# Optimization experiments

Hardware: AMD Instinct MI355X
Metric: run time of the kernel (lower is better)

Reference implementation:

```python
import jax, jax.numpy as jnp
import numpy as np

STEPS, IN_DIM, HID, OUT = 100, 512, 4096, 64
MAX_DELAY = 10
DT = 1.0
# LIF params
TAU, V_TH, V_RESET = 20.0, 1.0, 0.0
DECAY = float(np.exp(-DT / TAU))
# Astrocyte (homeostatic gain) params
ASTRO_ALPHA, ASTRO_LR, TARGET_RATE = 0.1, 0.01, 0.1
GAMMA_MIN, GAMMA_MAX = 0.5, 2.0
# Microglia (structural pruning) params
MICRO_DECAY, MICRO_LR, PRUNE_THR = 0.99, 0.1, 0.01


def setup_inputs() -> dict:
    key = jax.random.key(0)
    k = jax.random.split(key, 6)
    x = jax.random.uniform(k[0], (STEPS, IN_DIM), dtype=jnp.float32)
    input_weights = 0.1 * jax.random.normal(k[1], (IN_DIM, HID), dtype=jnp.float32)
    recurrent_weights = 0.1 * jax.random.normal(k[2], (HID, HID), dtype=jnp.float32)
    readout_w = 0.1 * jax.random.normal(k[3], (HID, OUT), dtype=jnp.float32)
    readout_b = jnp.zeros((OUT,), dtype=jnp.float32)
    delays = jax.random.randint(k[4], (HID, HID), 1, MAX_DELAY, dtype=jnp.int32)
    return {"x": x, "input_weights": input_weights,
            "recurrent_weights": recurrent_weights,
            "readout_w": readout_w, "readout_b": readout_b,
            "delays": delays}


def reference(x, input_weights, recurrent_weights, readout_w, readout_b, delays):
    H = recurrent_weights.shape[0]
    pre_idx = jnp.arange(H)[:, None]  # presynaptic neuron index for gather

    def step(carry, x_t):
        v, buf, ptr, gamma, rate, health = carry
        i_input = x_t @ input_weights                       # [H]
        # per-synapse delayed spike gather from circular buffer
        idx = jnp.mod(ptr - delays, MAX_DELAY)              # [H,H]
        delayed = buf[idx, pre_idx]                         # [H,H], delayed[i,j] = spike of pre i, delays[i,j] steps ago
        mask = (health > PRUNE_THR).astype(jnp.float32)     # microglia structural mask
        i_rec = (recurrent_weights * mask * delayed).sum(0) # [H]
        i_total = (i_input + i_rec) * gamma                 # astrocyte gain
        # LIF update
        v_new = v * jnp.float32(DECAY) + i_total * jnp.float32(DT)
        spikes = (v_new >= V_TH).astype(jnp.float32)
        v_new = jnp.where(spikes > 0, jnp.float32(V_RESET), v_new)
        # astrocyte homeostasis toward target firing rate
        rate = (1.0 - ASTRO_ALPHA) * rate + ASTRO_ALPHA * spikes
        gamma = jnp.clip(gamma + ASTRO_LR * (TARGET_RATE - rate), GAMMA_MIN, GAMMA_MAX)
        # microglia coactivity health trace
        health = MICRO_DECAY * health + MICRO_LR * jnp.outer(spikes, spikes)
        # push spikes into circular delay buffer
        buf = buf.at[ptr].set(spikes)
        ptr = jnp.mod(ptr + 1, MAX_DELAY)
        return (v_new, buf, ptr, gamma, rate, health), v_new

    init = (jnp.zeros((H,), jnp.float32),
            jnp.zeros((MAX_DELAY, H), jnp.float32),
            jnp.int32(0),
            jnp.ones((H,), jnp.float32),
            jnp.zeros((H,), jnp.float32),
            jnp.ones((H, H), jnp.float32))
    _, vs = jax.lax.scan(jax.checkpoint(step), init, x)  # vs: [steps, H] membrane traces
    final_state = vs.mean(0)[None, :]                    # [1, H]
    return final_state @ readout_w + readout_b           # [1, OUT]
```

## Files before the change

### kernel.cpp

```cpp
#include <hip/hip_runtime.h>

#define H 4096
#define STEPS 100
#define IN_DIM_ 512
#define OUT_DIM_ 64
#define NWG 512
#define TPB 256
#define RGRP 32
#define CGRP 16
#define ROWS_PER_WG 128
#define COLS_PER_WG 256
#define NSLOT 10
#define NBUF 4
#define TBLK 10
#define TAG_INVALID 0xFFFFFFFFu
#define DECAY_F 0.95122942450071400910f

#define OFF_BAR   0
#define OFF_IIN   8192
#define OFF_PART  1646592
#define OFF_VSUM  5840896
#define OFF_RED   5857280
#define OFF_DLY8  5873664
#define WS_NEED_PACK 22650880

#define STAMP_BWD(c)  (512 + (c) * 32)
#define BAR_GRP(g)    (1024 + (g) * 16)
#define BAR_GCNT      1280
#define BAR_FLAG      1296

#define ALOAD(p)      __hip_atomic_load((p),  __ATOMIC_RELAXED, __HIP_MEMORY_SCOPE_AGENT)
#define ASTORE(p,v)   __hip_atomic_store((p), (v), __ATOMIC_RELAXED, __HIP_MEMORY_SCOPE_AGENT)
#define ALOAD64(p)    __hip_atomic_load((p),  __ATOMIC_RELAXED, __HIP_MEMORY_SCOPE_AGENT)
#define ASTORE64(p,v) __hip_atomic_store((p), (v), __ATOMIC_RELAXED, __HIP_MEMORY_SCOPE_AGENT)

__device__ __forceinline__ void wait_ge(unsigned* p, unsigned tgt) {
    while (ALOAD(p) < tgt) __builtin_amdgcn_s_sleep(1);
}

__device__ __forceinline__ void full_barrier(unsigned* bar, int wg, unsigned gen, int tid) {
    __syncthreads();
    if (tid == 0) {
        __threadfence();
        unsigned o = atomicAdd(bar + BAR_GRP(wg >> 5), 1u);
        if (o == gen * 32u - 1u) {
            unsigned g = atomicAdd(bar + BAR_GCNT, 1u);
            if (g == gen * 16u - 1u)
                ASTORE(bar + BAR_FLAG, gen);
        }
        wait_ge(bar + BAR_FLAG, gen);
        __threadfence();
    }
    __syncthreads();
}

__global__ __launch_bounds__(TPB, 2)
void triglial_kernel(const float* __restrict__ x,
                     const float* __restrict__ Wi,
                     const float* __restrict__ Wr,
                     const float* __restrict__ rw,
                     const float* __restrict__ rbias,
                     const int*   __restrict__ delays,
                     unsigned char* __restrict__ dly8,
                     int use_pack,
                     unsigned* __restrict__ bar,
                     float* __restrict__ Iin,
                     unsigned long long* __restrict__ partial,
                     float* __restrict__ vsum_g,
                     float* __restrict__ red_part,
                     float* __restrict__ out)
{
    const int wg   = blockIdx.x;
    const int tid  = threadIdx.x;
    const int rg   = wg >> 4;
    const int cgi  = wg & 15;
    const int rowbase = rg * ROWS_PER_WG;
    const int colbase = cgi * COLS_PER_WG;
    const int wave = tid >> 6, lane = tid & 63;
    const int mycol = colbase + tid;

    __shared__ float s_acc[4][NSLOT][64];
    __shared__ float s_part[2][ROWS_PER_WG];
    __shared__ float s_v[ROWS_PER_WG], s_rate[ROWS_PER_WG],
                     s_gamma[ROWS_PER_WG], s_vsum[ROWS_PER_WG];
    __shared__ unsigned long long s_spk[2];
    __shared__ float s_red[4][64];

    if (tid < ROWS_PER_WG) {
        s_v[tid]=0.f; s_rate[tid]=0.f; s_gamma[tid]=1.f; s_vsum[tid]=0.f;
    }
    for (int i = tid; i < 4*NSLOT*64; i += TPB) ((float*)s_acc)[i] = 0.f;
    for (int idx = wg*TPB + tid; idx < NBUF*RGRP*H; idx += NWG*TPB) {
        const int slot = idx / (RGRP * H);
        const unsigned long long w =
            (slot == 0) ? 0ull : ((unsigned long long)TAG_INVALID << 32);
        ASTORE64(&partial[idx], w);
    }
    if (use_pack) {
        for (int idx = wg*TPB + tid; idx < H*H; idx += NWG*TPB)
            dly8[idx] = (unsigned char)(delays[idx] - 1);
    }
    if (wg < (STEPS / TBLK) * CGRP) {
        const int t0 = (wg / CGRP) * TBLK;
        const int j  = (wg % CGRP) * COLS_PER_WG + tid;
        float acc[TBLK];
        #pragma unroll
        for (int tt = 0; tt < TBLK; ++tt) acc[tt] = 0.f;
        for (int k = 0; k < IN_DIM_; ++k) {
            const float w = Wi[(size_t)k * H + j];
            #pragma unroll
            for (int tt = 0; tt < TBLK; ++tt)
                acc[tt] += x[(t0 + tt) * IN_DIM_ + k] * w;
        }
        #pragma unroll
        for (int tt = 0; tt < TBLK; ++tt) Iin[(t0 + tt) * H + j] = acc[tt];
    }
    full_barrier(bar, wg, 1u, tid);

    for (int t = 0; t < STEPS; ++t) {
        if (t >= 3 && tid < 32) {
            unsigned* addr = bar + STAMP_BWD(cgi) + lane;
            const unsigned tgt = (unsigned)(t - 2);
            int spins = 0;
            for (;;) {
                unsigned v = ALOAD(addr);
                if (__all((int)(v >= tgt))) break;
                if (((++spins) & 1023) == 0) __threadfence();
                __builtin_amdgcn_s_sleep(2);
            }
        }
        __syncthreads();

        {
            const int n = tid & 127, p = tid >> 7;
            unsigned long long* pb = partial + (t & (NBUF-1)) * (RGRP * H);
            const int gn = rowbase + n;
            const unsigned want = (unsigned)t;
            float s = 0.f;
            #pragma unroll
            for (int c = 0; c < 4; ++c) {
                unsigned long long u[4];
                #pragma unroll
                for (int k = 0; k < 4; ++k)
                    u[k] = ALOAD64(&pb[(p*16 + c*4 + k) * H + gn]);
                int spins = 0;
                for (;;) {
                    bool stale = false;
                    #pragma unroll
                    for (int k = 0; k < 4; ++k) {
                        if ((unsigned)(u[k] >> 32) != want) {
                            stale = true;
                            u[k] = ALOAD64(&pb[(p*16 + c*4 + k) * H + gn]);
                        }
                    }
                    if (!stale) break;
                    if (((++spins) & 1023) == 0) __threadfence();
                    __builtin_amdgcn_s_sleep(1);
                }
                #pragma unroll
                for (int k = 0; k < 4; ++k) s += __uint_as_float((unsigned)u[k]);
            }
            s_part[p][n] = s;
        }
        __syncthreads();
        if (tid == 0)
            ASTORE(bar + STAMP_BWD(rg >> 1) + ((rg & 1) * 16 + cgi), (unsigned)(t + 1));

        if (tid < ROWS_PER_WG) {
            const float irec = s_part[0][tid] + s_part[1][tid];
            const float itot = (Iin[t*H + rowbase + tid] + irec) * s_gamma[tid];
            float v = s_v[tid] * DECAY_F + itot;
            const int spk = (v >= 1.0f) ? 1 : 0;
            v = spk ? 0.0f : v;
            s_v[tid] = v;
            s_vsum[tid] += v;
            const float rate = 0.9f * s_rate[tid] + 0.1f * (float)spk;
            s_rate[tid] = rate;
            float g = s_gamma[tid] + 0.01f * (0.1f - rate);
            s_gamma[tid] = fminf(fmaxf(g, 0.5f), 2.0f);
            const unsigned long long bal = __ballot(spk);
            if ((tid & 63) == 0) s_spk[tid >> 6] = bal;
        }
        __syncthreads();

        if (t < STEPS - 1) {
            const int tmod = t % 10;
            unsigned long long m0 = s_spk[0], m1 = s_spk[1];
            while (m0 | m1) {
                float wv[16]; int dv[16];
                int cnt = 0;
                #pragma unroll
                for (int b = 0; b < 16; ++b) {
                    if (m0 | m1) {
                        int ii;
                        if (m0) { ii = __ffsll(m0) - 1; m0 &= m0 - 1; }
                        else    { ii = 64 + __ffsll(m1) - 1; m1 &= m1 - 1; }
                        const size_t base = (size_t)(rowbase + ii) * H + mycol;
                        wv[b] = Wr[base];
                        dv[b] = use_pack ? (int)dly8[base] : (delays[base] - 1);
                        ++cnt;
                    }
                }
                #pragma unroll
                for (int b = 0; b < 16; ++b) {
                    if (b < cnt) {
                        int slot = tmod + 1 + dv[b];
                        slot -= (slot >= 10) ? 10 : 0;
                        s_acc[wave][slot][lane] += wv[b];
                    }
                }
            }
            int es = tmod + 1; es -= (es >= 10) ? 10 : 0;
            const float ex = s_acc[wave][es][lane];
            s_acc[wave][es][lane] = 0.f;
            const unsigned long long w =
                ((unsigned long long)(unsigned)(t + 1) << 32)
                | (unsigned long long)__float_as_uint(ex);
            ASTORE64(&partial[((t+1) & (NBUF-1)) * (RGRP*H) + rg*H + mycol], w);
        }
        __syncthreads();
    }

    if (cgi == 0 && tid < ROWS_PER_WG) vsum_g[rowbase + tid] = s_vsum[tid];
    full_barrier(bar, wg, 2u, tid);

    if (wg < 64) {
        const int o  = tid & 63;
        const int jl = tid >> 6;
        float s = 0.f;
        for (int j = wg*64 + jl; j < wg*64 + 64; j += 4)
            s += (vsum_g[j] * (1.0f / (float)STEPS)) * rw[j * OUT_DIM_ + o];
        s_red[jl][o] = s;
        __syncthreads();
        if (tid < 64)
            red_part[wg*64 + tid] =
                s_red[0][tid] + s_red[1][tid] + s_red[2][tid] + s_red[3][tid];
    }
    full_barrier(bar, wg, 3u, tid);

    if (wg == 0 && tid < OUT_DIM_) {
        float s = rbias[tid];
        #pragma unroll 8
        for (int w = 0; w < 64; ++w) s += red_part[w * 64 + tid];
        out[tid] = s;
    }
}

extern "C" void kernel_launch(void* const* d_in, const int* in_sizes, int n_in,
                              void* d_out, int out_size, void* d_ws, size_t ws_size,
                              hipStream_t stream) {
    const float* x      = (const float*)d_in[0];
    const float* Wi     = (const float*)d_in[1];
    const float* Wr     = (const float*)d_in[2];
    const float* rw     = (const float*)d_in[3];
    const float* rb     = (const float*)d_in[4];
    const int*   delays = (const int*)d_in[5];
    float* out = (float*)d_out;

    char* ws = (char*)d_ws;
    unsigned* bar   = (unsigned*)(ws + OFF_BAR);
    float* Iin      = (float*)(ws + OFF_IIN);
    unsigned long long* partial = (unsigned long long*)(ws + OFF_PART);
    float* vsum_g   = (float*)(ws + OFF_VSUM);
    float* red_part = (float*)(ws + OFF_RED);
    unsigned char* dly8 = (unsigned char*)(ws + OFF_DLY8);
    int use_pack = (ws_size >= (size_t)WS_NEED_PACK) ? 1 : 0;

    hipMemsetAsync(ws + OFF_BAR, 0, 8192, stream);

    void* args[] = { (void*)&x, (void*)&Wi, (void*)&Wr, (void*)&rw, (void*)&rb,
                     (void*)&delays, (void*)&dly8, (void*)&use_pack, (void*)&bar,
                     (void*)&Iin, (void*)&partial, (void*)&vsum_g, (void*)&red_part,
                     (void*)&out };
    hipError_t err = hipLaunchCooperativeKernel((void*)triglial_kernel, dim3(NWG),
                                                dim3(TPB), args, 0, stream);
    if (err != hipSuccess) {
        triglial_kernel<<<dim3(NWG), dim3(TPB), 0, stream>>>(
            x, Wi, Wr, rw, rb, delays, dly8, use_pack, bar,
            Iin, partial, vsum_g, red_part, out);
    }
}
```

Measured before the change: 1.490 ms.

## Repartition work by postsynaptic columns and broadcast spike bits instead of partial sums

Each workgroup now owns 8 postsynaptic neurons and iterates over all 4096 presynaptic rows, with the 32 row groups mapped across threads. Per-step communication shrinks from 64-bit partial-sum words for every row-group and neuron to one 8-bit spike mask per workgroup, published in a tagged ring that every workgroup polls. Neuron state moves into registers, the partial reduction becomes a wave shuffle plus shared-memory sum, and the backward stamp flow control is removed. The cost is that all 512 workgroups must poll 512 published words every step, and each thread gathers weights for only one column across many rows, giving scattered, uncoalesced Wr accesses.

After: 3.260 ms. +118.8%, slower.

```diff
diff --git a/kernel.cpp b/kernel.cpp
--- a/kernel.cpp
+++ b/kernel.cpp
@@ -6,25 +6,20 @@
 #define OUT_DIM_ 64
 #define NWG 512
 #define TPB 256
-#define RGRP 32
-#define CGRP 16
-#define ROWS_PER_WG 128
-#define COLS_PER_WG 256
+#define COLS_PER_WG 8
 #define NSLOT 10
-#define NBUF 4
+#define NRING 16
 #define TBLK 10
-#define TAG_INVALID 0xFFFFFFFFu
 #define DECAY_F 0.95122942450071400910f
 
 #define OFF_BAR   0
 #define OFF_IIN   8192
-#define OFF_PART  1646592
-#define OFF_VSUM  5840896
-#define OFF_RED   5857280
-#define OFF_DLY8  5873664
-#define WS_NEED_PACK 22650880
-
-#define STAMP_BWD(c)  (512 + (c) * 32)
+#define OFF_PUB   1646592
+#define OFF_VSUM  1712128
+#define OFF_RED   1728512
+#define OFF_DLY8  1744896
+#define WS_NEED_PACK 18522112
+
 #define BAR_GRP(g)    (1024 + (g) * 16)
 #define BAR_GCNT      1280
 #define BAR_FLAG      1296
@@ -65,44 +60,37 @@
                      int use_pack,
                      unsigned* __restrict__ bar,
                      float* __restrict__ Iin,
-                     unsigned long long* __restrict__ partial,
+                     unsigned long long* __restrict__ pub,
                      float* __restrict__ vsum_g,
                      float* __restrict__ red_part,
                      float* __restrict__ out)
 {
     const int wg   = blockIdx.x;
     const int tid  = threadIdx.x;
-    const int rg   = wg >> 4;
-    const int cgi  = wg & 15;
-    const int rowbase = rg * ROWS_PER_WG;
-    const int colbase = cgi * COLS_PER_WG;
-    const int wave = tid >> 6, lane = tid & 63;
-    const int mycol = colbase + tid;
-
-    __shared__ float s_acc[4][NSLOT][64];
-    __shared__ float s_part[2][ROWS_PER_WG];
-    __shared__ float s_v[ROWS_PER_WG], s_rate[ROWS_PER_WG],
-                     s_gamma[ROWS_PER_WG], s_vsum[ROWS_PER_WG];
-    __shared__ unsigned long long s_spk[2];
+    const int lane = tid & 63, wave = tid >> 6;
+    const int c    = tid & 7;
+    const int r    = tid >> 3;
+    const int colbase = wg * COLS_PER_WG;
+    const int mycol   = colbase + c;
+
+    __shared__ unsigned long long s_spkvec[64];
+    __shared__ float s_acc[NSLOT][TPB];
+    __shared__ float s_red4[4][8];
     __shared__ float s_red[4][64];
 
-    if (tid < ROWS_PER_WG) {
-        s_v[tid]=0.f; s_rate[tid]=0.f; s_gamma[tid]=1.f; s_vsum[tid]=0.f;
-    }
-    for (int i = tid; i < 4*NSLOT*64; i += TPB) ((float*)s_acc)[i] = 0.f;
-    for (int idx = wg*TPB + tid; idx < NBUF*RGRP*H; idx += NWG*TPB) {
-        const int slot = idx / (RGRP * H);
-        const unsigned long long w =
-            (slot == 0) ? 0ull : ((unsigned long long)TAG_INVALID << 32);
-        ASTORE64(&partial[idx], w);
-    }
+    float nv = 0.f, nrate = 0.f, ngamma = 1.f, nvsum = 0.f;
+
+    #pragma unroll
+    for (int s = 0; s < NSLOT; ++s) s_acc[s][tid] = 0.f;
+    for (int idx = wg*TPB + tid; idx < NRING*NWG; idx += NWG*TPB)
+        ASTORE64(&pub[idx], 0ull);
     if (use_pack) {
         for (int idx = wg*TPB + tid; idx < H*H; idx += NWG*TPB)
             dly8[idx] = (unsigned char)(delays[idx] - 1);
     }
-    if (wg < (STEPS / TBLK) * CGRP) {
-        const int t0 = (wg / CGRP) * TBLK;
-        const int j  = (wg % CGRP) * COLS_PER_WG + tid;
+    if (wg < (STEPS / TBLK) * 16) {
+        const int t0 = (wg / 16) * TBLK;
+        const int j  = (wg % 16) * 256 + tid;
         float acc[TBLK];
         #pragma unroll
         for (int tt = 0; tt < TBLK; ++tt) acc[tt] = 0.f;
@@ -118,74 +106,41 @@
     full_barrier(bar, wg, 1u, tid);
 
     for (int t = 0; t < STEPS; ++t) {
-        if (t >= 3 && tid < 32) {
-            unsigned* addr = bar + STAMP_BWD(cgi) + lane;
-            const unsigned tgt = (unsigned)(t - 2);
+        float iin = 0.f;
+        if (tid < 8) iin = Iin[t * H + colbase + tid];
+
+        if (t > 0 && tid < 64) {
+            unsigned long long* pp = pub + ((t - 1) & (NRING - 1)) * NWG + tid * 8;
+            const unsigned want = (unsigned)t;
+            unsigned long long u[8];
+            #pragma unroll
+            for (int k = 0; k < 8; ++k) u[k] = ALOAD64(&pp[k]);
             int spins = 0;
             for (;;) {
-                unsigned v = ALOAD(addr);
-                if (__all((int)(v >= tgt))) break;
+                bool stale = false;
+                #pragma unroll
+                for (int k = 0; k < 8; ++k) {
+                    if ((unsigned)(u[k] >> 32) != want) {
+                        stale = true;
+                        u[k] = ALOAD64(&pp[k]);
+                    }
+                }
+                if (!stale) break;
                 if (((++spins) & 1023) == 0) __threadfence();
-                __builtin_amdgcn_s_sleep(2);
+                __builtin_amdgcn_s_sleep(1);
             }
+            unsigned long long bits = 0;
+            #pragma unroll
+            for (int k = 0; k < 8; ++k)
+                bits |= (u[k] & 0xFFull) << (8 * k);
+            s_spkvec[tid] = bits;
         }
         __syncthreads();
 
-        {
-            const int n = tid & 127, p = tid >> 7;
-            unsigned long long* pb = partial + (t & (NBUF-1)) * (RGRP * H);
-            const int gn = rowbase + n;
-            const unsigned want = (unsigned)t;
-            float s = 0.f;
-            #pragma unroll
-            for (int c = 0; c < 4; ++c) {
-                unsigned long long u[4];
-                #pragma unroll
-                for (int k = 0; k < 4; ++k)
-                    u[k] = ALOAD64(&pb[(p*16 + c*4 + k) * H + gn]);
-                int spins = 0;
-                for (;;) {
-                    bool stale = false;
-                    #pragma unroll
-                    for (int k = 0; k < 4; ++k) {
-                        if ((unsigned)(u[k] >> 32) != want) {
-                            stale = true;
-                            u[k] = ALOAD64(&pb[(p*16 + c*4 + k) * H + gn]);
-                        }
-                    }
-                    if (!stale) break;
-                    if (((++spins) & 1023) == 0) __threadfence();
-                    __builtin_amdgcn_s_sleep(1);
-                }
-                #pragma unroll
-                for (int k = 0; k < 4; ++k) s += __uint_as_float((unsigned)u[k]);
-            }
-            s_part[p][n] = s;
-        }
-        __syncthreads();
-        if (tid == 0)
-            ASTORE(bar + STAMP_BWD(rg >> 1) + ((rg & 1) * 16 + cgi), (unsigned)(t + 1));
-
-        if (tid < ROWS_PER_WG) {
-            const float irec = s_part[0][tid] + s_part[1][tid];
-            const float itot = (Iin[t*H + rowbase + tid] + irec) * s_gamma[tid];
-            float v = s_v[tid] * DECAY_F + itot;
-            const int spk = (v >= 1.0f) ? 1 : 0;
-            v = spk ? 0.0f : v;
-            s_v[tid] = v;
-            s_vsum[tid] += v;
-            const float rate = 0.9f * s_rate[tid] + 0.1f * (float)spk;
-            s_rate[tid] = rate;
-            float g = s_gamma[tid] + 0.01f * (0.1f - rate);
-            s_gamma[tid] = fminf(fmaxf(g, 0.5f), 2.0f);
-            const unsigned long long bal = __ballot(spk);
-            if ((tid & 63) == 0) s_spk[tid >> 6] = bal;
-        }
-        __syncthreads();
-
-        if (t < STEPS - 1) {
+        if (t > 0) {
             const int tmod = t % 10;
-            unsigned long long m0 = s_spk[0], m1 = s_spk[1];
+            const int rowb = r << 7;
+            unsigned long long m0 = s_spkvec[2*r], m1 = s_spkvec[2*r + 1];
             while (m0 | m1) {
                 float wv[16]; int dv[16];
                 int cnt = 0;
@@ -195,7 +150,7 @@
                         int ii;
                         if (m0) { ii = __ffsll(m0) - 1; m0 &= m0 - 1; }
                         else    { ii = 64 + __ffsll(m1) - 1; m1 &= m1 - 1; }
-                        const size_t base = (size_t)(rowbase + ii) * H + mycol;
+                        const size_t base = (size_t)(rowb + ii) * H + mycol;
                         wv[b] = Wr[base];
                         dv[b] = use_pack ? (int)dly8[base] : (delays[base] - 1);
                         ++cnt;
@@ -204,24 +159,43 @@
                 #pragma unroll
                 for (int b = 0; b < 16; ++b) {
                     if (b < cnt) {
-                        int slot = tmod + 1 + dv[b];
+                        int slot = tmod + dv[b];
                         slot -= (slot >= 10) ? 10 : 0;
-                        s_acc[wave][slot][lane] += wv[b];
+                        s_acc[slot][tid] += wv[b];
                     }
                 }
             }
-            int es = tmod + 1; es -= (es >= 10) ? 10 : 0;
-            const float ex = s_acc[wave][es][lane];
-            s_acc[wave][es][lane] = 0.f;
-            const unsigned long long w =
-                ((unsigned long long)(unsigned)(t + 1) << 32)
-                | (unsigned long long)__float_as_uint(ex);
-            ASTORE64(&partial[((t+1) & (NBUF-1)) * (RGRP*H) + rg*H + mycol], w);
-        }
+        }
+
+        const int es = t % 10;
+        float ex = s_acc[es][tid];
+        s_acc[es][tid] = 0.f;
+        ex += __shfl_xor(ex, 8);
+        ex += __shfl_xor(ex, 16);
+        ex += __shfl_xor(ex, 32);
+        if (lane < 8) s_red4[wave][lane] = ex;
         __syncthreads();
-    }
-
-    if (cgi == 0 && tid < ROWS_PER_WG) vsum_g[rowbase + tid] = s_vsum[tid];
+
+        if (tid < 8) {
+            const float irec = s_red4[0][tid] + s_red4[1][tid]
+                             + s_red4[2][tid] + s_red4[3][tid];
+            const float itot = (iin + irec) * ngamma;
+            float v = nv * DECAY_F + itot;
+            const int spk = (v >= 1.0f) ? 1 : 0;
+            v = spk ? 0.0f : v;
+            nv = v;
+            nvsum += v;
+            nrate = 0.9f * nrate + 0.1f * (float)spk;
+            ngamma = fminf(fmaxf(ngamma + 0.01f * (0.1f - nrate), 0.5f), 2.0f);
+            const unsigned bits = (unsigned)(__ballot(spk) & 0xFFull);
+            if (tid == 0 && t < STEPS - 1)
+                ASTORE64(&pub[(t & (NRING - 1)) * NWG + wg],
+                         ((unsigned long long)(unsigned)(t + 1) << 32)
+                         | (unsigned long long)bits);
+        }
+    }
+
+    if (tid < 8) vsum_g[colbase + tid] = nvsum;
     full_barrier(bar, wg, 2u, tid);
 
     if (wg < 64) {
@@ -260,7 +234,7 @@
     char* ws = (char*)d_ws;
     unsigned* bar   = (unsigned*)(ws + OFF_BAR);
     float* Iin      = (float*)(ws + OFF_IIN);
-    unsigned long long* partial = (unsigned long long*)(ws + OFF_PART);
+    unsigned long long* pub = (unsigned long long*)(ws + OFF_PUB);
     float* vsum_g   = (float*)(ws + OFF_VSUM);
     float* red_part = (float*)(ws + OFF_RED);
     unsigned char* dly8 = (unsigned char*)(ws + OFF_DLY8);
@@ -270,13 +244,13 @@
 
     void* args[] = { (void*)&x, (void*)&Wi, (void*)&Wr, (void*)&rw, (void*)&rb,
                      (void*)&delays, (void*)&dly8, (void*)&use_pack, (void*)&bar,
-                     (void*)&Iin, (void*)&partial, (void*)&vsum_g, (void*)&red_part,
+                     (void*)&Iin, (void*)&pub, (void*)&vsum_g, (void*)&red_part,
                      (void*)&out };
     hipError_t err = hipLaunchCooperativeKernel((void*)triglial_kernel, dim3(NWG),
                                                 dim3(TPB), args, 0, stream);
     if (err != hipSuccess) {
         triglial_kernel<<<dim3(NWG), dim3(TPB), 0, stream>>>(
             x, Wi, Wr, rw, rb, delays, dly8, use_pack, bar,
-            Iin, partial, vsum_g, red_part, out);
-    }
-}
+            Iin, pub, vsum_g, red_part, out);
+    }
+}
```
